# Kernel tuning notes

Measured on AMD Instinct MI355X. Metric: run time of the kernel, lower is better.

Reference implementation:

```python
import jax, jax.numpy as jnp
import numpy as np

ORDER = 3  # polynomial filter order


def _sketch_conv(x, A, W, b, coeffs):
    # z = A @ (x W + b); out = sum_d coeffs[d-1] * z**d  (Horner-free power accumulation)
    z = A @ (x @ W + b)            # [N, out_c]
    p = z
    acc = coeffs[0] * z
    for d in range(1, ORDER):      # small fixed loop over polynomial order
        p = p * z
        acc = acc + coeffs[d] * p
    return acc


def setup_inputs() -> dict:
    key = jax.random.key(0)
    ks = jax.random.split(key, 12)
    N, C_IN, C_H, C_OUT = 8192, 128, 64, 40
    nf_mats = jax.random.normal(ks[0], (N, C_IN), dtype=jnp.float32)
    # scale by 1/sqrt(N) so polynomial powers stay O(1)
    conv_mats = jax.random.normal(ks[1], (N, N), dtype=jnp.float32) / np.float32(np.sqrt(N))
    def lin(k, fi, fo):
        kw, kb = jax.random.split(k)
        W = jax.random.normal(kw, (fi, fo), dtype=jnp.float32) / np.float32(np.sqrt(fi))
        b = jax.random.normal(kb, (fo,), dtype=jnp.float32) * np.float32(0.01)
        return W, b
    W1, b1 = lin(ks[2], C_IN, C_H)
    W2, b2 = lin(ks[3], C_H, C_H)
    W3, b3 = lin(ks[4], C_H, C_OUT)
    base = jnp.array([1.0, 0.0, 0.0], dtype=jnp.float32)
    c1 = base + jax.random.normal(ks[5], (ORDER,), dtype=jnp.float32) * 0.05
    c2 = base + jax.random.normal(ks[6], (ORDER,), dtype=jnp.float32) * 0.05
    c3 = base + jax.random.normal(ks[7], (ORDER,), dtype=jnp.float32) * 0.05
    return {"nf_mats": nf_mats, "conv_mats": conv_mats,
            "W1": W1, "b1": b1, "c1": c1,
            "W2": W2, "b2": b2, "c2": c2,
            "W3": W3, "b3": b3, "c3": c3}


def reference(nf_mats, conv_mats, W1, b1, c1, W2, b2, c2, W3, b3, c3):
    # SketchGCN eval-mode forward: batchnorm=False, dropout inactive.
    x = _sketch_conv(nf_mats, conv_mats, W1, b1, c1)      # first layer
    x = x + _sketch_conv(x, conv_mats, W2, b2, c2)        # residual middle layer
    return _sketch_conv(x, conv_mats, W3, b3, c3)         # output layer
```

## Files before the change

kernel.cpp:

```cpp
#include <hip/hip_runtime.h>
#include <stdint.h>

typedef __bf16 bf16x8 __attribute__((ext_vector_type(8)));
typedef float f32x4 __attribute__((ext_vector_type(4)));

using gvoid = const __attribute__((address_space(1))) void;
using lvoid = __attribute__((address_space(3))) void;

__device__ __forceinline__ unsigned short f2bf(float f) {
    union { float f; unsigned u; } x; x.f = f;
    unsigned u = x.u;
    u += 0x7FFFu + ((u >> 16) & 1u);
    return (unsigned short)(u >> 16);
}
__device__ __forceinline__ unsigned pack2(float lo, float hi) {
    return ((unsigned)f2bf(hi) << 16) | (unsigned)f2bf(lo);
}

__global__ __launch_bounds__(256)
void convert_small(const float* __restrict__ Amat, unsigned short* __restrict__ Abf,
                   const float* __restrict__ X, const float* __restrict__ W,
                   const float* __restrict__ b, unsigned short* __restrict__ Yt) {
    __shared__ float Xs[32 * 129];
    __shared__ float Ws[128 * 64];
    __shared__ float bs[64];
    const int t = threadIdx.x;

    if (blockIdx.x < 2048) {
        const int n8 = 8192 * 8192 / 8;
        int idx = blockIdx.x * 256 + t;
        const float4* in4 = (const float4*)Amat;
        uint4* out8 = (uint4*)Abf;
        for (int i = idx; i < n8; i += 2048 * 256) {
            float4 a = in4[2 * i], c = in4[2 * i + 1];
            uint4 o;
            o.x = pack2(a.x, a.y);
            o.y = pack2(a.z, a.w);
            o.z = pack2(c.x, c.y);
            o.w = pack2(c.z, c.w);
            out8[i] = o;
        }
        return;
    }

    const int i0 = (blockIdx.x - 2048) * 32;
    for (int e = t; e < 32 * 128; e += 256) {
        int r = e >> 7, c = e & 127;
        Xs[r * 129 + c] = X[(size_t)(i0 + r) * 128 + c];
    }
    for (int e = t; e < 128 * 64; e += 256) Ws[e] = W[e];
    if (t < 64) bs[t] = b[t];
    __syncthreads();

    const int i = t & 31;
    const int jg = t >> 5;
    float acc[8];
#pragma unroll
    for (int jj = 0; jj < 8; ++jj) acc[jj] = 0.0f;
    for (int k = 0; k < 128; ++k) {
        float xv = Xs[i * 129 + k];
        const float4* wr = (const float4*)&Ws[k * 64 + jg * 8];
        float4 w0 = wr[0], w1 = wr[1];
        acc[0] += xv * w0.x; acc[1] += xv * w0.y;
        acc[2] += xv * w0.z; acc[3] += xv * w0.w;
        acc[4] += xv * w1.x; acc[5] += xv * w1.y;
        acc[6] += xv * w1.z; acc[7] += xv * w1.w;
    }
#pragma unroll
    for (int jj = 0; jj < 8; ++jj) {
        int j = jg * 8 + jj;
        Yt[(size_t)j * 8192 + i0 + i] = f2bf(acc[jj] + bs[j]);
    }
}

__global__ __launch_bounds__(256, 4)
void big_gemm(const unsigned short* __restrict__ Ab,
              const unsigned short* __restrict__ Yt,
              float* __restrict__ P) {
    __shared__ unsigned short As[2][64 * 64];
    const int t = threadIdx.x;
    const int lane = t & 63, wid = t >> 6;
    const int lane15 = lane & 15, lane4 = lane >> 4;
    const int wm = wid >> 1, wn = wid & 1;
    const int row0 = blockIdx.x * 64;
    const int kbase = blockIdx.y * 1024;

    const unsigned short* bP[2][2];
#pragma unroll
    for (int n = 0; n < 2; ++n)
#pragma unroll
        for (int ks = 0; ks < 2; ++ks)
            bP[n][ks] = Yt + (size_t)(wn * 32 + n * 16 + lane15) * 8192 +
                        kbase + ks * 32 + lane4 * 8;

    f32x4 acc[2][2];
    const f32x4 z4 = {0.f, 0.f, 0.f, 0.f};
#pragma unroll
    for (int m = 0; m < 2; ++m)
#pragma unroll
        for (int n = 0; n < 2; ++n) acc[m][n] = z4;

    bf16x8 breg[2][2][2];

    auto stageA = [&](int slot, int kt) {
#pragma unroll
        for (int ii = 0; ii < 2; ++ii) {
            int p = ii * 256 + wid * 64 + lane;
            int r = p >> 3;
            int c = (p & 7) ^ (r & 7);
            const unsigned short* gp = Ab + (size_t)(row0 + r) * 8192 + (kt + c * 8);
            unsigned short* lp = &As[slot][(ii * 256 + wid * 64) * 8];
            __builtin_amdgcn_global_load_lds((gvoid*)gp, (lvoid*)lp, 16, 0, 0);
        }
    };

    stageA(0, kbase);
#pragma unroll
    for (int n = 0; n < 2; ++n)
#pragma unroll
        for (int ks = 0; ks < 2; ++ks)
            breg[0][n][ks] = *(const bf16x8*)(bP[n][ks]);

#pragma unroll
    for (int tt = 0; tt < 16; ++tt) {
        if (tt + 1 < 16) {
            stageA((tt + 1) & 1, kbase + (tt + 1) * 64);
#pragma unroll
            for (int n = 0; n < 2; ++n)
#pragma unroll
                for (int ks = 0; ks < 2; ++ks)
                    breg[(tt + 1) & 1][n][ks] =
                        *(const bf16x8*)(bP[n][ks] + (tt + 1) * 64);
            asm volatile("s_waitcnt vmcnt(6)\n\ts_barrier" ::: "memory");
        } else {
            asm volatile("s_waitcnt vmcnt(0)\n\ts_barrier" ::: "memory");
        }
#pragma unroll
        for (int ks = 0; ks < 2; ++ks) {
            bf16x8 af[2];
#pragma unroll
            for (int m = 0; m < 2; ++m) {
                int r = wm * 32 + m * 16 + lane15;
                int c = ks * 4 + lane4;
                af[m] = *(const bf16x8*)&As[tt & 1][((r << 3) | (c ^ (r & 7))) << 3];
            }
#pragma unroll
            for (int m = 0; m < 2; ++m)
#pragma unroll
                for (int n = 0; n < 2; ++n)
                    acc[m][n] = __builtin_amdgcn_mfma_f32_16x16x32_bf16(
                        af[m], breg[tt & 1][n][ks], acc[m][n], 0, 0, 0);
        }
        asm volatile("s_barrier" ::: "memory");
    }

    float* Po = P + (size_t)blockIdx.y * (8192 * 64);
#pragma unroll
    for (int m = 0; m < 2; ++m) {
        int r = row0 + wm * 32 + m * 16 + lane4 * 4;
#pragma unroll
        for (int n = 0; n < 2; ++n) {
            int cc = wn * 32 + n * 16 + lane15;
#pragma unroll
            for (int q = 0; q < 4; ++q)
                Po[(size_t)(r + q) * 64 + cc] = acc[m][n][q];
        }
    }
}

template <int MODE>
__global__ __launch_bounds__(256) void fused_reduce(const float* __restrict__ P,
                                                    const float* __restrict__ cf,
                                                    const float* __restrict__ Wn,
                                                    const float* __restrict__ bn,
                                                    int cout,
                                                    float* __restrict__ X1,
                                                    unsigned short* __restrict__ Yt) {
    __shared__ float Xs[64 * 33];
    __shared__ float Ws[64 * 64];
    __shared__ float bs[64];
    const int t = threadIdx.x;
    const int i0 = blockIdx.x * 32;
    const int NT4 = 8192 * 64 / 4;
    const float4* P4 = (const float4*)P;
    float4* X14 = (float4*)X1;

    for (int e = t; e < 64 * 64; e += 256) {
        int k = e >> 6, j = e & 63;
        Ws[e] = (j < cout) ? Wn[k * cout + j] : 0.0f;
    }
    if (t < 64) bs[t] = (t < cout) ? bn[t] : 0.0f;
    const float c0 = cf[0], c1 = cf[1], c2 = cf[2];

#pragma unroll
    for (int s = 0; s < 2; ++s) {
        int e4 = s * 256 + t;
        int i = e4 >> 4, jc = e4 & 15;
        int base4 = (i0 + i) * 16 + jc;
        float4 z = {0.f, 0.f, 0.f, 0.f};
#pragma unroll
        for (int ks = 0; ks < 8; ++ks) {
            float4 p = P4[(size_t)ks * NT4 + base4];
            z.x += p.x; z.y += p.y; z.z += p.z; z.w += p.w;
        }
        float4 v;
        v.x = z.x * (c0 + z.x * (c1 + z.x * c2));
        v.y = z.y * (c0 + z.y * (c1 + z.y * c2));
        v.z = z.z * (c0 + z.z * (c1 + z.z * c2));
        v.w = z.w * (c0 + z.w * (c1 + z.w * c2));
        if (MODE == 0) {
            X14[base4] = v;
        } else {
            float4 xr = X14[base4];
            v.x += xr.x; v.y += xr.y; v.z += xr.z; v.w += xr.w;
        }
        Xs[(jc * 4 + 0) * 33 + i] = v.x;
        Xs[(jc * 4 + 1) * 33 + i] = v.y;
        Xs[(jc * 4 + 2) * 33 + i] = v.z;
        Xs[(jc * 4 + 3) * 33 + i] = v.w;
    }
    __syncthreads();

    const int i = t & 31;
    const int jg = t >> 5;
    float acc[8];
#pragma unroll
    for (int jj = 0; jj < 8; ++jj) acc[jj] = 0.0f;
    for (int k = 0; k < 64; ++k) {
        float xv = Xs[k * 33 + i];
        const float4* wr = (const float4*)&Ws[k * 64 + jg * 8];
        float4 w0 = wr[0], w1 = wr[1];
        acc[0] += xv * w0.x; acc[1] += xv * w0.y;
        acc[2] += xv * w0.z; acc[3] += xv * w0.w;
        acc[4] += xv * w1.x; acc[5] += xv * w1.y;
        acc[6] += xv * w1.z; acc[7] += xv * w1.w;
    }
#pragma unroll
    for (int jj = 0; jj < 8; ++jj) {
        int j = jg * 8 + jj;
        Yt[(size_t)j * 8192 + i0 + i] = f2bf(acc[jj] + bs[j]);
    }
}

__global__ void reduce_out(const float* __restrict__ P, const float* __restrict__ cf,
                           float* __restrict__ out) {
    int e4 = blockIdx.x * 256 + threadIdx.x;
    const int NT4 = 8192 * 64 / 4;
    const float4* P4 = (const float4*)P;
    float4 z = {0.f, 0.f, 0.f, 0.f};
#pragma unroll
    for (int ks = 0; ks < 8; ++ks) {
        float4 p = P4[(size_t)ks * NT4 + e4];
        z.x += p.x; z.y += p.y; z.z += p.z; z.w += p.w;
    }
    float c0 = cf[0], c1 = cf[1], c2 = cf[2];
    float4 v;
    v.x = z.x * (c0 + z.x * (c1 + z.x * c2));
    v.y = z.y * (c0 + z.y * (c1 + z.y * c2));
    v.z = z.z * (c0 + z.z * (c1 + z.z * c2));
    v.w = z.w * (c0 + z.w * (c1 + z.w * c2));
    int i = e4 >> 4, jc = e4 & 15;
    if (jc < 10) ((float4*)out)[i * 10 + jc] = v;
}

extern "C" void kernel_launch(void* const* d_in, const int* in_sizes, int n_in,
                              void* d_out, int out_size, void* d_ws, size_t ws_size,
                              hipStream_t stream) {
    const float* nf   = (const float*)d_in[0];
    const float* Amat = (const float*)d_in[1];
    const float* W1   = (const float*)d_in[2];
    const float* b1   = (const float*)d_in[3];
    const float* c1   = (const float*)d_in[4];
    const float* W2   = (const float*)d_in[5];
    const float* b2   = (const float*)d_in[6];
    const float* c2   = (const float*)d_in[7];
    const float* W3   = (const float*)d_in[8];
    const float* b3   = (const float*)d_in[9];
    const float* c3   = (const float*)d_in[10];
    float* out = (float*)d_out;

    char* ws = (char*)d_ws;
    unsigned short* Abf = (unsigned short*)(ws);
    unsigned short* Yt  = (unsigned short*)(ws + 134217728);
    float* X1           = (float*)(ws + 135266304);
    float* Pp           = (float*)(ws + 137363456);

    convert_small<<<2304, 256, 0, stream>>>(Amat, Abf, nf, W1, b1, Yt);

    big_gemm<<<dim3(128, 8), 256, 0, stream>>>(Abf, Yt, Pp);
    fused_reduce<0><<<256, 256, 0, stream>>>(Pp, c1, W2, b2, 64, X1, Yt);

    big_gemm<<<dim3(128, 8), 256, 0, stream>>>(Abf, Yt, Pp);
    fused_reduce<1><<<256, 256, 0, stream>>>(Pp, c2, W3, b3, 40, X1, Yt);

    big_gemm<<<dim3(128, 8), 256, 0, stream>>>(Abf, Yt, Pp);
    reduce_out<<<512, 256, 0, stream>>>(Pp, c3, out);
}
```

Measured before the change: 236.2 us.

## Stage B tile through LDS and halve GEMM row tile to 32

The A·Y GEMM now stages the 64x64 B tile (the transposed Yt operand) into LDS with global_load_lds alongside A, instead of having each wave load its B fragments straight into registers. The block shrinks to 128 threads covering 32 rows, and the grid doubles to 256x8. Each wave now covers all 32 rows and its own half of the columns. The aim is more resident blocks and parallelism on this memory-bound GEMM, and less duplicated per-wave B loading. The cost is extra LDS traffic and one more shared buffer per block.

```diff
diff --git a/kernel.cpp b/kernel.cpp
--- a/kernel.cpp
+++ b/kernel.cpp
@@ -73,25 +73,17 @@
     }
 }
 
-__global__ __launch_bounds__(256, 4)
+__global__ __launch_bounds__(128, 3)
 void big_gemm(const unsigned short* __restrict__ Ab,
               const unsigned short* __restrict__ Yt,
               float* __restrict__ P) {
-    __shared__ unsigned short As[2][64 * 64];
+    __shared__ unsigned short As[2][32 * 64];
+    __shared__ unsigned short Bs[2][64 * 64];
     const int t = threadIdx.x;
     const int lane = t & 63, wid = t >> 6;
     const int lane15 = lane & 15, lane4 = lane >> 4;
-    const int wm = wid >> 1, wn = wid & 1;
-    const int row0 = blockIdx.x * 64;
+    const int row0 = blockIdx.x * 32;
     const int kbase = blockIdx.y * 1024;
-
-    const unsigned short* bP[2][2];
-#pragma unroll
-    for (int n = 0; n < 2; ++n)
-#pragma unroll
-        for (int ks = 0; ks < 2; ++ks)
-            bP[n][ks] = Yt + (size_t)(wn * 32 + n * 16 + lane15) * 8192 +
-                        kbase + ks * 32 + lane4 * 8;
 
     f32x4 acc[2][2];
     const f32x4 z4 = {0.f, 0.f, 0.f, 0.f};
@@ -100,56 +92,57 @@
 #pragma unroll
         for (int n = 0; n < 2; ++n) acc[m][n] = z4;
 
-    bf16x8 breg[2][2][2];
-
-    auto stageA = [&](int slot, int kt) {
+    auto stage = [&](int slot, int kt) {
 #pragma unroll
         for (int ii = 0; ii < 2; ++ii) {
-            int p = ii * 256 + wid * 64 + lane;
+            int p = ii * 128 + t;
             int r = p >> 3;
             int c = (p & 7) ^ (r & 7);
             const unsigned short* gp = Ab + (size_t)(row0 + r) * 8192 + (kt + c * 8);
-            unsigned short* lp = &As[slot][(ii * 256 + wid * 64) * 8];
+            unsigned short* lp = &As[slot][(ii * 128 + wid * 64) * 8];
             __builtin_amdgcn_global_load_lds((gvoid*)gp, (lvoid*)lp, 16, 0, 0);
         }
+#pragma unroll
+        for (int ii = 0; ii < 4; ++ii) {
+            int q = ii * 128 + t;
+            int n = q >> 3;
+            int c = (q & 7) ^ (n & 7);
+            const unsigned short* gp = Yt + (size_t)n * 8192 + (kt + c * 8);
+            unsigned short* lp = &Bs[slot][(ii * 128 + wid * 64) * 8];
+            __builtin_amdgcn_global_load_lds((gvoid*)gp, (lvoid*)lp, 16, 0, 0);
+        }
     };
 
-    stageA(0, kbase);
-#pragma unroll
-    for (int n = 0; n < 2; ++n)
-#pragma unroll
-        for (int ks = 0; ks < 2; ++ks)
-            breg[0][n][ks] = *(const bf16x8*)(bP[n][ks]);
-
-#pragma unroll
-    for (int tt = 0; tt < 16; ++tt) {
-        if (tt + 1 < 16) {
-            stageA((tt + 1) & 1, kbase + (tt + 1) * 64);
-#pragma unroll
-            for (int n = 0; n < 2; ++n)
-#pragma unroll
-                for (int ks = 0; ks < 2; ++ks)
-                    breg[(tt + 1) & 1][n][ks] =
-                        *(const bf16x8*)(bP[n][ks] + (tt + 1) * 64);
+    stage(0, kbase);
+    const int NIT = 16;
+    for (int tt = 0; tt < NIT; ++tt) {
+        if (tt + 1 < NIT) {
+            stage((tt + 1) & 1, kbase + (tt + 1) * 64);
             asm volatile("s_waitcnt vmcnt(6)\n\ts_barrier" ::: "memory");
         } else {
             asm volatile("s_waitcnt vmcnt(0)\n\ts_barrier" ::: "memory");
         }
 #pragma unroll
         for (int ks = 0; ks < 2; ++ks) {
-            bf16x8 af[2];
+            bf16x8 af[2], bfr[2];
 #pragma unroll
             for (int m = 0; m < 2; ++m) {
-                int r = wm * 32 + m * 16 + lane15;
+                int r = m * 16 + lane15;
                 int c = ks * 4 + lane4;
                 af[m] = *(const bf16x8*)&As[tt & 1][((r << 3) | (c ^ (r & 7))) << 3];
             }
 #pragma unroll
+            for (int n = 0; n < 2; ++n) {
+                int rn = wid * 32 + n * 16 + lane15;
+                int c = ks * 4 + lane4;
+                bfr[n] = *(const bf16x8*)&Bs[tt & 1][((rn << 3) | (c ^ (rn & 7))) << 3];
+            }
+#pragma unroll
             for (int m = 0; m < 2; ++m)
 #pragma unroll
                 for (int n = 0; n < 2; ++n)
                     acc[m][n] = __builtin_amdgcn_mfma_f32_16x16x32_bf16(
-                        af[m], breg[tt & 1][n][ks], acc[m][n], 0, 0, 0);
+                        af[m], bfr[n], acc[m][n], 0, 0, 0);
         }
         asm volatile("s_barrier" ::: "memory");
     }
@@ -157,10 +150,10 @@
     float* Po = P + (size_t)blockIdx.y * (8192 * 64);
 #pragma unroll
     for (int m = 0; m < 2; ++m) {
-        int r = row0 + wm * 32 + m * 16 + lane4 * 4;
+        int r = row0 + m * 16 + lane4 * 4;
 #pragma unroll
         for (int n = 0; n < 2; ++n) {
-            int cc = wn * 32 + n * 16 + lane15;
+            int cc = wid * 32 + n * 16 + lane15;
 #pragma unroll
             for (int q = 0; q < 4; ++q)
                 Po[(size_t)(r + q) * 64 + cc] = acc[m][n][q];
@@ -287,12 +280,12 @@
 
     convert_small<<<2304, 256, 0, stream>>>(Amat, Abf, nf, W1, b1, Yt);
 
-    big_gemm<<<dim3(128, 8), 256, 0, stream>>>(Abf, Yt, Pp);
+    big_gemm<<<dim3(256, 8), 128, 0, stream>>>(Abf, Yt, Pp);
     fused_reduce<0><<<256, 256, 0, stream>>>(Pp, c1, W2, b2, 64, X1, Yt);
 
-    big_gemm<<<dim3(128, 8), 256, 0, stream>>>(Abf, Yt, Pp);
+    big_gemm<<<dim3(256, 8), 128, 0, stream>>>(Abf, Yt, Pp);
     fused_reduce<1><<<256, 256, 0, stream>>>(Pp, c2, W3, b3, 40, X1, Yt);
 
-    big_gemm<<<dim3(128, 8), 256, 0, stream>>>(Abf, Yt, Pp);
+    big_gemm<<<dim3(256, 8), 128, 0, stream>>>(Abf, Yt, Pp);
     reduce_out<<<512, 256, 0, stream>>>(Pp, c3, out);
 }
```

After: 216.5 us. -8.3%, faster.
